# Kernel optimization log

Hardware: AMD Instinct MI355X
Metric: run time of the kernel (lower is better)

The kernel has to match this reference:

```python
import jax, jax.numpy as jnp
import numpy as np

N_NODES = 100000
N_EDGES = 1600000
H_FEATS = 64


def setup_inputs() -> dict:
    key = jax.random.key(0)
    k_h, k_src, k_dst, k_w1, k_b1, k_w2, k_b2 = jax.random.split(key, 7)
    h = jax.random.normal(k_h, (N_NODES, H_FEATS), dtype=jnp.float32)
    src = jax.random.randint(k_src, (N_EDGES,), 0, N_NODES, dtype=jnp.int64)
    dst = jax.random.randint(k_dst, (N_EDGES,), 0, N_NODES, dtype=jnp.int64)
    # Linear params (torch Linear: y = x @ W.T + b). Store as [in, out] for jnp.
    lim1 = 1.0 / np.sqrt(2 * H_FEATS)
    W1 = jax.random.uniform(k_w1, (2 * H_FEATS, H_FEATS), minval=-lim1, maxval=lim1, dtype=jnp.float32)
    b1 = jax.random.uniform(k_b1, (H_FEATS,), minval=-lim1, maxval=lim1, dtype=jnp.float32)
    lim2 = 1.0 / np.sqrt(H_FEATS)
    W2 = jax.random.uniform(k_w2, (H_FEATS, 1), minval=-lim2, maxval=lim2, dtype=jnp.float32)
    b2 = jax.random.uniform(k_b2, (1,), minval=-lim2, maxval=lim2, dtype=jnp.float32)
    return {"h": h, "src": src, "dst": dst, "W1": W1, "b1": b1, "W2": W2, "b2": b2}


def reference(h, src, dst, W1, b1, W2, b2):
    # Gather src/dst node features per edge, avoid materializing the concat by
    # splitting W1 into the src-half and dst-half of the contraction.
    W1s, W1d = W1[:H_FEATS], W1[H_FEATS:]            # each [h, h]
    h_src = h[src]                                    # [E, h]
    h_dst = h[dst]                                    # [E, h]
    hidden = jax.nn.relu(h_src @ W1s + h_dst @ W1d + b1)  # [E, h]
    score = (hidden @ W2 + b2)[:, 0]                  # [E]
    return score
```

## Files before the change

kernel.cpp:

```cpp
#include <hip/hip_runtime.h>
#include <hip/hip_fp16.h>


#define HF 64

__global__ __launch_bounds__(512) void node_proj_kernel(
    const float* __restrict__ h, const float* __restrict__ W1,
    const float* __restrict__ b1, __half* __restrict__ P,
    __half* __restrict__ Q, int n_nodes)
{
    const int lane = threadIdx.x & 63;
    const int wave = __builtin_amdgcn_readfirstlane(threadIdx.x >> 6);
    const int c0   = wave * 16;
    const bool isQ = c0 >= 64;
    const int ccol = c0 & 63;

    const float* wbase = W1 + (isQ ? (64 * 64) : 0) + ccol;
    __half* const outh = (isQ ? Q : P) + ccol;

    const int n = blockIdx.x * 64 + lane;
    const bool valid = (n < n_nodes);
    const int nc = valid ? n : (n_nodes - 1);
    const float4* hrow = (const float4*)(h + (size_t)nc * HF);

    float acc[16];
    #pragma unroll
    for (int j = 0; j < 16; ++j) acc[j] = isQ ? 0.0f : b1[ccol + j];

    #pragma unroll
    for (int k4 = 0; k4 < 16; ++k4) {
        const float4 v = hrow[k4];
        const float* w0 = wbase + (k4 * 4 + 0) * 64;
        const float* w1 = wbase + (k4 * 4 + 1) * 64;
        const float* w2 = wbase + (k4 * 4 + 2) * 64;
        const float* w3 = wbase + (k4 * 4 + 3) * 64;
        #pragma unroll
        for (int j = 0; j < 16; ++j) {
            acc[j] = fmaf(v.x, w0[j], acc[j]);
            acc[j] = fmaf(v.y, w1[j], acc[j]);
            acc[j] = fmaf(v.z, w2[j], acc[j]);
            acc[j] = fmaf(v.w, w3[j], acc[j]);
        }
    }

    if (valid) {
        union { uint4 u[2]; __half2 hh[8]; } pk;
        #pragma unroll
        for (int j = 0; j < 8; ++j)
            pk.hh[j] = __floats2half2_rn(acc[j * 2], acc[j * 2 + 1]);
        __half* base = outh + (size_t)n * HF;
        *(uint4*)(base)     = pk.u[0];
        *(uint4*)(base + 8) = pk.u[1];
    }
}

__device__ __forceinline__ float dot8_relu(uint4 pv, uint4 qv, float4 wa, float4 wb) {
    const __half2* ph = (const __half2*)&pv;
    const __half2* qh = (const __half2*)&qv;
    const float2 p0 = __half22float2(ph[0]), q0 = __half22float2(qh[0]);
    const float2 p1 = __half22float2(ph[1]), q1 = __half22float2(qh[1]);
    const float2 p2 = __half22float2(ph[2]), q2 = __half22float2(qh[2]);
    const float2 p3 = __half22float2(ph[3]), q3 = __half22float2(qh[3]);
    float acc = 0.f;
    acc = fmaf(fmaxf(p0.x + q0.x, 0.f), wa.x, acc);
    acc = fmaf(fmaxf(p0.y + q0.y, 0.f), wa.y, acc);
    acc = fmaf(fmaxf(p1.x + q1.x, 0.f), wa.z, acc);
    acc = fmaf(fmaxf(p1.y + q1.y, 0.f), wa.w, acc);
    acc = fmaf(fmaxf(p2.x + q2.x, 0.f), wb.x, acc);
    acc = fmaf(fmaxf(p2.y + q2.y, 0.f), wb.y, acc);
    acc = fmaf(fmaxf(p3.x + q3.x, 0.f), wb.z, acc);
    acc = fmaf(fmaxf(p3.y + q3.y, 0.f), wb.w, acc);
    return acc;
}

__device__ __forceinline__ float red8(float v) {
    v += __shfl_xor(v, 4, 8);
    v += __shfl_xor(v, 2, 8);
    v += __shfl_xor(v, 1, 8);
    return v;
}

__global__ __launch_bounds__(256) void edge_score_kernel(
    const __half* __restrict__ P, const __half* __restrict__ Q,
    const int* __restrict__ src, const int* __restrict__ dst,
    const float* __restrict__ W2, const float* __restrict__ b2,
    float* __restrict__ out, int n_edges)
{
    const int tid   = blockIdx.x * 256 + threadIdx.x;
    const int sub   = threadIdx.x & 7;
    const int group = tid >> 3;
    const int j0    = sub * 8;
    const int e0    = group * 8;
    if (e0 >= n_edges) return;

    const float4 w2a = *(const float4*)(W2 + j0);
    const float4 w2b = *(const float4*)(W2 + j0 + 4);
    const float bias2 = b2[0];

    if (e0 + 8 <= n_edges) {
        const int4 sA = *(const int4*)(src + e0);
        const int4 sB = *(const int4*)(src + e0 + 4);
        const int4 dA = *(const int4*)(dst + e0);
        const int4 dB = *(const int4*)(dst + e0 + 4);

        const uint4 p0 = *(const uint4*)(P + (size_t)sA.x * HF + j0);
        const uint4 p1 = *(const uint4*)(P + (size_t)sA.y * HF + j0);
        const uint4 p2 = *(const uint4*)(P + (size_t)sA.z * HF + j0);
        const uint4 p3 = *(const uint4*)(P + (size_t)sA.w * HF + j0);
        const uint4 p4 = *(const uint4*)(P + (size_t)sB.x * HF + j0);
        const uint4 p5 = *(const uint4*)(P + (size_t)sB.y * HF + j0);
        const uint4 p6 = *(const uint4*)(P + (size_t)sB.z * HF + j0);
        const uint4 p7 = *(const uint4*)(P + (size_t)sB.w * HF + j0);
        const uint4 q0 = *(const uint4*)(Q + (size_t)dA.x * HF + j0);
        const uint4 q1 = *(const uint4*)(Q + (size_t)dA.y * HF + j0);
        const uint4 q2 = *(const uint4*)(Q + (size_t)dA.z * HF + j0);
        const uint4 q3 = *(const uint4*)(Q + (size_t)dA.w * HF + j0);
        const uint4 q4 = *(const uint4*)(Q + (size_t)dB.x * HF + j0);
        const uint4 q5 = *(const uint4*)(Q + (size_t)dB.y * HF + j0);
        const uint4 q6 = *(const uint4*)(Q + (size_t)dB.z * HF + j0);
        const uint4 q7 = *(const uint4*)(Q + (size_t)dB.w * HF + j0);

        float s0 = red8(dot8_relu(p0, q0, w2a, w2b));
        float s1 = red8(dot8_relu(p1, q1, w2a, w2b));
        float s2 = red8(dot8_relu(p2, q2, w2a, w2b));
        float s3 = red8(dot8_relu(p3, q3, w2a, w2b));
        float s4 = red8(dot8_relu(p4, q4, w2a, w2b));
        float s5 = red8(dot8_relu(p5, q5, w2a, w2b));
        float s6 = red8(dot8_relu(p6, q6, w2a, w2b));
        float s7 = red8(dot8_relu(p7, q7, w2a, w2b));

        if (sub == 0) {
            *(float4*)(out + e0)     = make_float4(s0 + bias2, s1 + bias2,
                                                   s2 + bias2, s3 + bias2);
            *(float4*)(out + e0 + 4) = make_float4(s4 + bias2, s5 + bias2,
                                                   s6 + bias2, s7 + bias2);
        }
    } else {
        for (int e = e0; e < n_edges; ++e) {
            const int s = src[e];
            const int d = dst[e];
            const uint4 pv = *(const uint4*)(P + (size_t)s * HF + j0);
            const uint4 qv = *(const uint4*)(Q + (size_t)d * HF + j0);
            float sc = red8(dot8_relu(pv, qv, w2a, w2b));
            if (sub == 0) out[e] = sc + bias2;
        }
    }
}

extern "C" void kernel_launch(void* const* d_in, const int* in_sizes, int n_in,
                              void* d_out, int out_size, void* d_ws, size_t ws_size,
                              hipStream_t stream) {
    const float* h   = (const float*)d_in[0];
    const int*   src = (const int*)d_in[1];
    const int*   dst = (const int*)d_in[2];
    const float* W1  = (const float*)d_in[3];
    const float* b1  = (const float*)d_in[4];
    const float* W2  = (const float*)d_in[5];
    const float* b2  = (const float*)d_in[6];
    float* out = (float*)d_out;

    const int n_nodes = in_sizes[0] / HF;
    const int n_edges = in_sizes[1];

    __half* P = (__half*)d_ws;
    __half* Q = P + (size_t)n_nodes * HF;

    const int nblocks1 = (n_nodes + 63) / 64;
    node_proj_kernel<<<nblocks1, 512, 0, stream>>>(h, W1, b1, P, Q, n_nodes);

    const int ngroups  = (n_edges + 7) / 8;
    const int nblocks2 = (ngroups + 31) / 32;
    edge_score_kernel<<<nblocks2, 256, 0, stream>>>(P, Q, src, dst, W2, b2, out, n_edges);
}
```

Measured before the change: 166.1 us.

## Stage node feature tile in LDS and compute two nodes per thread

The node projection kernel now loads a 128-node tile of h into padded shared memory with coalesced float4 loads, instead of having each lane read its own row straight from global memory. Each thread then computes two nodes, so every W1 weight load is reused across two accumulator sets. The goal is to cut redundant global traffic for h and W1 in the first kernel. In exchange it uses about 33KB of LDS per block and twice the accumulator registers, and the edge kernel, which likely dominates total time, is unchanged.

```diff
diff --git a/kernel.cpp b/kernel.cpp
--- a/kernel.cpp
+++ b/kernel.cpp
@@ -2,53 +2,89 @@
 #include <hip/hip_fp16.h>
 
 
-#define HF 64
+#define HF  64
+#define PAD 65
+#define TN  128
 
 __global__ __launch_bounds__(512) void node_proj_kernel(
     const float* __restrict__ h, const float* __restrict__ W1,
     const float* __restrict__ b1, __half* __restrict__ P,
     __half* __restrict__ Q, int n_nodes)
 {
-    const int lane = threadIdx.x & 63;
-    const int wave = __builtin_amdgcn_readfirstlane(threadIdx.x >> 6);
+    __shared__ float hs[TN * PAD];
+
+    const int tid  = threadIdx.x;
+    const int lane = tid & 63;
+    const int wave = __builtin_amdgcn_readfirstlane(tid >> 6);
     const int c0   = wave * 16;
     const bool isQ = c0 >= 64;
     const int ccol = c0 & 63;
 
-    const float* wbase = W1 + (isQ ? (64 * 64) : 0) + ccol;
+    const float* wbase = W1 + (isQ ? (HF * HF) : 0) + ccol;
     __half* const outh = (isQ ? Q : P) + ccol;
 
-    const int n = blockIdx.x * 64 + lane;
-    const bool valid = (n < n_nodes);
-    const int nc = valid ? n : (n_nodes - 1);
-    const float4* hrow = (const float4*)(h + (size_t)nc * HF);
-
-    float acc[16];
+    const int n0 = blockIdx.x * TN;
+
+    {
+        const int nrow  = (n_nodes - n0 < TN) ? (n_nodes - n0) : TN;
+        const int maxf4 = nrow * 16;
+        const float4* hv = (const float4*)(h + (size_t)n0 * HF);
+        #pragma unroll
+        for (int it = 0; it < 4; ++it) {
+            const int idx  = tid + it * 512;
+            const int cidx = (idx < maxf4) ? idx : 0;
+            const float4 v = hv[cidx];
+            const int row = idx >> 4;
+            const int c4  = (idx & 15) * 4;
+            float* dst = &hs[row * PAD + c4];
+            dst[0] = v.x; dst[1] = v.y; dst[2] = v.z; dst[3] = v.w;
+        }
+    }
+    __syncthreads();
+
+    float acc0[16], acc1[16];
     #pragma unroll
-    for (int j = 0; j < 16; ++j) acc[j] = isQ ? 0.0f : b1[ccol + j];
-
-    #pragma unroll
-    for (int k4 = 0; k4 < 16; ++k4) {
-        const float4 v = hrow[k4];
-        const float* w0 = wbase + (k4 * 4 + 0) * 64;
-        const float* w1 = wbase + (k4 * 4 + 1) * 64;
-        const float* w2 = wbase + (k4 * 4 + 2) * 64;
-        const float* w3 = wbase + (k4 * 4 + 3) * 64;
+    for (int j = 0; j < 16; ++j) {
+        const float b = isQ ? 0.0f : b1[ccol + j];
+        acc0[j] = b; acc1[j] = b;
+    }
+
+    const float* r0 = &hs[lane * PAD];
+    const float* r1 = &hs[(lane + 64) * PAD];
+
+    #pragma unroll 4
+    for (int k2 = 0; k2 < 32; ++k2) {
+        const float a0 = r0[2 * k2], a1 = r0[2 * k2 + 1];
+        const float c0v = r1[2 * k2], c1v = r1[2 * k2 + 1];
+        const float* wA = wbase + (2 * k2) * HF;
+        const float* wB = wbase + (2 * k2 + 1) * HF;
         #pragma unroll
         for (int j = 0; j < 16; ++j) {
-            acc[j] = fmaf(v.x, w0[j], acc[j]);
-            acc[j] = fmaf(v.y, w1[j], acc[j]);
-            acc[j] = fmaf(v.z, w2[j], acc[j]);
-            acc[j] = fmaf(v.w, w3[j], acc[j]);
-        }
-    }
-
-    if (valid) {
+            const float wa = wA[j], wb = wB[j];
+            acc0[j] = fmaf(a0, wa, acc0[j]);
+            acc0[j] = fmaf(a1, wb, acc0[j]);
+            acc1[j] = fmaf(c0v, wa, acc1[j]);
+            acc1[j] = fmaf(c1v, wb, acc1[j]);
+        }
+    }
+
+    const int n_a = n0 + lane;
+    const int n_b = n0 + lane + 64;
+    if (n_a < n_nodes) {
         union { uint4 u[2]; __half2 hh[8]; } pk;
         #pragma unroll
         for (int j = 0; j < 8; ++j)
-            pk.hh[j] = __floats2half2_rn(acc[j * 2], acc[j * 2 + 1]);
-        __half* base = outh + (size_t)n * HF;
+            pk.hh[j] = __floats2half2_rn(acc0[2 * j], acc0[2 * j + 1]);
+        __half* base = outh + (size_t)n_a * HF;
+        *(uint4*)(base)     = pk.u[0];
+        *(uint4*)(base + 8) = pk.u[1];
+    }
+    if (n_b < n_nodes) {
+        union { uint4 u[2]; __half2 hh[8]; } pk;
+        #pragma unroll
+        for (int j = 0; j < 8; ++j)
+            pk.hh[j] = __floats2half2_rn(acc1[2 * j], acc1[2 * j + 1]);
+        __half* base = outh + (size_t)n_b * HF;
         *(uint4*)(base)     = pk.u[0];
         *(uint4*)(base + 8) = pk.u[1];
     }
@@ -165,7 +201,7 @@
     __half* P = (__half*)d_ws;
     __half* Q = P + (size_t)n_nodes * HF;
 
-    const int nblocks1 = (n_nodes + 63) / 64;
+    const int nblocks1 = (n_nodes + TN - 1) / TN;
     node_proj_kernel<<<nblocks1, 512, 0, stream>>>(h, W1, b1, P, Q, n_nodes);
 
     const int ngroups  = (n_edges + 7) / 8;
```

After: 156.2 us. 1.06x faster.
